# Performance work log

Measured on AMD Instinct MI355X. Metric: run time of the kernel, lower is better.

Reference implementation:

```python
import jax, jax.numpy as jnp
import numpy as np

B, T, IN_DIM = 128, 4096, 13
UNITS, MOTOR = 64, 6
LAYERS = [35, 23, 6]   # AutoNCP(64, 6): inter / command / motor neurons
_SPLITS = [35, 58]     # cumulative layer boundaries inside the 64-unit state


def setup_inputs() -> dict:
    keys = iter(jax.random.split(jax.random.key(0), 64))
    def rn(shape, s=0.1):
        return jax.random.normal(next(keys), shape, dtype=jnp.float32) * s
    inp = {"x": jax.random.normal(next(keys), (B, T, IN_DIM), dtype=jnp.float32)}
    # mixed-memory LSTM cell (ncps: input_map has bias, recurrent_map does not)
    inp["lstm_wi"] = rn((4 * UNITS, IN_DIM))
    inp["lstm_wh"] = rn((4 * UNITS, UNITS))
    inp["lstm_b"] = rn((4 * UNITS,))
    # wired CfC layers: ff1/ff2/time_a/time_b acting on concat([input, h])
    in_dims = [IN_DIM] + LAYERS[:-1]
    for i, (d, h) in enumerate(zip(in_dims, LAYERS)):
        for nm in ("w1", "w2", "wa", "wb"):
            inp[f"cfc{i}_{nm}"] = rn((h, d + h))
        for nm in ("b1", "b2", "ba", "bb"):
            inp[f"cfc{i}_{nm}"] = rn((h,))
    inp["gyro_w1"] = rn((32, MOTOR)); inp["gyro_b1"] = rn((32,))
    inp["gyro_w2"] = rn((3, 32));     inp["gyro_b2"] = rn((3,))
    inp["acc_w1"] = rn((32, MOTOR));  inp["acc_b1"] = rn((32,))
    inp["acc_w2"] = rn((3, 32));      inp["acc_b2"] = rn((3,))
    inp["unc_w1"] = rn((16, MOTOR));  inp["unc_b1"] = rn((16,))
    inp["unc_w2"] = rn((6, 16));      inp["unc_b2"] = rn((6,))
    return inp


def _cfc_step(inp, h, p):
    """ncps CfCCell, mode='default', no backbone, ts = 1.0."""
    W1, b1, W2, b2, Wa, ba, Wb, bb = p
    z = jnp.concatenate([inp, h], axis=-1)            # (B, in+hid)
    ff1 = jnp.tanh(z @ W1.T + b1)
    ff2 = jnp.tanh(z @ W2.T + b2)
    t = jax.nn.sigmoid((z @ Wa.T + ba) + (z @ Wb.T + bb))  # t_a*ts + t_b, ts==1
    return ff1 * (1.0 - t) + t * ff2


def reference(x, lstm_wi, lstm_wh, lstm_b,
              cfc0_w1, cfc0_b1, cfc0_w2, cfc0_b2, cfc0_wa, cfc0_ba, cfc0_wb, cfc0_bb,
              cfc1_w1, cfc1_b1, cfc1_w2, cfc1_b2, cfc1_wa, cfc1_ba, cfc1_wb, cfc1_bb,
              cfc2_w1, cfc2_b1, cfc2_w2, cfc2_b2, cfc2_wa, cfc2_ba, cfc2_wb, cfc2_bb,
              gyro_w1, gyro_b1, gyro_w2, gyro_b2,
              acc_w1, acc_b1, acc_w2, acc_b2,
              unc_w1, unc_b1, unc_w2, unc_b2):
    layer_params = (
        (cfc0_w1, cfc0_b1, cfc0_w2, cfc0_b2, cfc0_wa, cfc0_ba, cfc0_wb, cfc0_bb),
        (cfc1_w1, cfc1_b1, cfc1_w2, cfc1_b2, cfc1_wa, cfc1_ba, cfc1_wb, cfc1_bb),
        (cfc2_w1, cfc2_b1, cfc2_w2, cfc2_b2, cfc2_wa, cfc2_ba, cfc2_wb, cfc2_bb),
    )

    def step(carry, xt):  # xt: (B, 13)
        h, c = carry
        # mixed-memory LSTM over the full 64-unit state (forget gate +1.0)
        zg = xt @ lstm_wi.T + lstm_b + h @ lstm_wh.T
        ia, ig, fg, og = jnp.split(zg, 4, axis=-1)
        c_new = c * jax.nn.sigmoid(fg + 1.0) + jnp.tanh(ia) * jax.nn.sigmoid(ig)
        h_lstm = jnp.tanh(c_new) * jax.nn.sigmoid(og)
        # wired CfC: inter -> command -> motor, each fed previous layer's output
        hs = jnp.split(h_lstm, _SPLITS, axis=-1)
        inp = xt
        new_hs = []
        for hi, p in zip(hs, layer_params):
            inp = _cfc_step(inp, hi, p)
            new_hs.append(inp)
        return (jnp.concatenate(new_hs, axis=-1), c_new), inp  # motor out (B,6)

    Bsz = x.shape[0]
    h0 = jnp.zeros((Bsz, UNITS), x.dtype)
    c0 = jnp.zeros((Bsz, UNITS), x.dtype)
    _, outs = jax.lax.scan(step, (h0, c0), jnp.swapaxes(x, 0, 1))
    cfc_out = jnp.swapaxes(outs, 0, 1)  # (B, T, 6)

    gyro = jnp.tanh(cfc_out @ gyro_w1.T + gyro_b1) @ gyro_w2.T + gyro_b2
    acc = jnp.tanh(cfc_out @ acc_w1.T + acc_b1) @ acc_w2.T + acc_b2
    pred = jnp.concatenate([gyro, acc], axis=-1)                      # (B, T, 6)
    unc = jax.nn.softplus(
        jax.nn.relu(cfc_out @ unc_w1.T + unc_b1) @ unc_w2.T + unc_b2)  # (B, T, 6)
    return pred, unc
```

## Files before the change

### kernel.cpp

```cpp
#include <hip/hip_runtime.h>
#include <math.h>

#define BATCH 128
#define TSTEPS 4096
#define INDIM 13


__device__ __forceinline__ float fsig(float x) {
    return __builtin_amdgcn_rcpf(1.f + __expf(-x));
}
__device__ __forceinline__ float ftanh(float x) {
    float s = fsig(x + x);
    return s + s - 1.f;
}
__device__ __forceinline__ float fsoftplus(float x) {
    return (x > 15.f) ? x : __logf(1.f + __expf(x));
}

__device__ __forceinline__ float qxor1(float v) {
    return __int_as_float(__builtin_amdgcn_update_dpp(
        0, __float_as_int(v), 0xB1, 0xF, 0xF, true));
}
__device__ __forceinline__ float qxor2(float v) {
    return __int_as_float(__builtin_amdgcn_update_dpp(
        0, __float_as_int(v), 0x4E, 0xF, 0xF, true));
}
__device__ __forceinline__ float sxor4(float v) {
    return __int_as_float(__builtin_amdgcn_ds_swizzle(
        __float_as_int(v), 0x101F));
}
#define BFLY8(a) { a += sxor4(a); a += qxor2(a); a += qxor1(a); }

#define FMA4(acc, W, q, zv) { acc += zv.x * W##_##q##_0; acc += zv.y * W##_##q##_1; \
                              acc += zv.z * W##_##q##_2; acc += zv.w * W##_##q##_3; }

__global__ __launch_bounds__(512, 2)
void rnn_kernel(const float* __restrict__ x,
                const float* __restrict__ lstm_wi, const float* __restrict__ lstm_wh,
                const float* __restrict__ lstm_b,
                const float* __restrict__ c0w1, const float* __restrict__ c0w2,
                const float* __restrict__ c0wa, const float* __restrict__ c0wb,
                const float* __restrict__ c0b1, const float* __restrict__ c0b2,
                const float* __restrict__ c0ba, const float* __restrict__ c0bb,
                const float* __restrict__ c1w1, const float* __restrict__ c1w2,
                const float* __restrict__ c1wa, const float* __restrict__ c1wb,
                const float* __restrict__ c1b1, const float* __restrict__ c1b2,
                const float* __restrict__ c1ba, const float* __restrict__ c1bb,
                const float* __restrict__ c2w1, const float* __restrict__ c2w2,
                const float* __restrict__ c2wa, const float* __restrict__ c2wb,
                const float* __restrict__ c2b1, const float* __restrict__ c2b2,
                const float* __restrict__ c2ba, const float* __restrict__ c2bb,
                float* __restrict__ out)
{
    const int bb = blockIdx.x;
    const int t  = threadIdx.x;
    const int k  = t & 7;
    const int u  = t >> 3;

    __shared__ __align__(16) float smem[256];
    float* zL = smem;
    float* z0 = smem + 96;
    float* z1 = smem + 160;
    float* z2 = smem + 224;

    const long xbase = (long)bb * TSTEPS * INDIM;
    const long obase = (long)bb * TSTEPS * 6;

    auto lwf = [&](int A, int c) -> float {
        int r = A * 64 + u;
        return (c < 13) ? lstm_wi[r * 13 + c]
             : (c < 77) ? lstm_wh[r * 64 + (c - 13)] : 0.f;
    };
#define DEF_WL(A,q) \
    float wl##A##_##q##_0 = lwf(A, 12*k + 4*q + 0); \
    float wl##A##_##q##_1 = lwf(A, 12*k + 4*q + 1); \
    float wl##A##_##q##_2 = lwf(A, 12*k + 4*q + 2); \
    float wl##A##_##q##_3 = lwf(A, 12*k + 4*q + 3);
    DEF_WL(0,0) DEF_WL(0,1) DEF_WL(0,2)
    DEF_WL(1,0) DEF_WL(1,1) DEF_WL(1,2)
    DEF_WL(2,0) DEF_WL(2,1) DEF_WL(2,2)
    DEF_WL(3,0) DEF_WL(3,1) DEF_WL(3,2)
#undef DEF_WL
    const float bL0 = lstm_b[u];
    const float bL1 = lstm_b[64 + u];
    const float bL2 = lstm_b[128 + u];
    const float bL3 = lstm_b[192 + u];

    const int grp  = (u < 35) ? 0 : (u < 58) ? 1 : 2;
    const int row  = (grp == 0) ? u : (grp == 1) ? (u - 35) : (u - 58);
    const int rl   = (grp == 0) ? 48 : (grp == 1) ? 58 : 29;
    const int clen = (grp == 2) ? 4 : 8;
    const int cb   = (grp == 2) ? 4 * k : 8 * k;
    const float *W0p, *W1p, *W2p, *W3p;
    float bC0, bC1, bC2, bC3;
    if (grp == 0) {
        W0p = c0w1 + row * 48; W1p = c0w2 + row * 48;
        W2p = c0wa + row * 48; W3p = c0wb + row * 48;
        bC0 = c0b1[row]; bC1 = c0b2[row]; bC2 = c0ba[row]; bC3 = c0bb[row];
    } else if (grp == 1) {
        W0p = c1w1 + row * 58; W1p = c1w2 + row * 58;
        W2p = c1wa + row * 58; W3p = c1wb + row * 58;
        bC0 = c1b1[row]; bC1 = c1b2[row]; bC2 = c1ba[row]; bC3 = c1bb[row];
    } else {
        W0p = c2w1 + row * 29; W1p = c2w2 + row * 29;
        W2p = c2wa + row * 29; W3p = c2wb + row * 29;
        bC0 = c2b1[row]; bC1 = c2b2[row]; bC2 = c2ba[row]; bC3 = c2bb[row];
    }
    auto cwf = [&](const float* W, int c) -> float {
        int cc = cb + c;
        return (c < clen && cc < rl) ? W[cc] : 0.f;
    };
#define DEF_WC(A,q) \
    float wc##A##_##q##_0 = cwf(W##A##p, 4*q + 0); \
    float wc##A##_##q##_1 = cwf(W##A##p, 4*q + 1); \
    float wc##A##_##q##_2 = cwf(W##A##p, 4*q + 2); \
    float wc##A##_##q##_3 = cwf(W##A##p, 4*q + 3);
    DEF_WC(0,0) DEF_WC(0,1)
    DEF_WC(1,0) DEF_WC(1,1)
    DEF_WC(2,0) DEF_WC(2,1)
    DEF_WC(3,0) DEF_WC(3,1)
#undef DEF_WC

    const bool pfl = (t >= 128 && t < 141);
    float creg = 0.f;

    if (t < 256) smem[t] = 0.f;
    __syncthreads();
    if (t < 13) zL[t] = x[xbase + t];
    __syncthreads();

    #pragma unroll 1
    for (int ts = 0; ts < TSTEPS; ++ts) {
        float xn = 0.f;
        if (pfl && (ts + 1) < TSTEPS)
            xn = x[xbase + (long)(ts + 1) * 13 + (t - 128)];
        if (t >= 256 && t < 269) z0[t - 256] = zL[t - 256];
        {
            const float4* zc = (const float4*)(zL + 12 * k);
            float4 q0 = zc[0], q1 = zc[1], q2 = zc[2];
            float a0 = 0.f, a1 = 0.f, a2 = 0.f, a3 = 0.f;
            FMA4(a0, wl0, 0, q0) FMA4(a0, wl0, 1, q1) FMA4(a0, wl0, 2, q2)
            FMA4(a1, wl1, 0, q0) FMA4(a1, wl1, 1, q1) FMA4(a1, wl1, 2, q2)
            FMA4(a2, wl2, 0, q0) FMA4(a2, wl2, 1, q1) FMA4(a2, wl2, 2, q2)
            FMA4(a3, wl3, 0, q0) FMA4(a3, wl3, 1, q1) FMA4(a3, wl3, 2, q2)
            BFLY8(a0) BFLY8(a1) BFLY8(a2) BFLY8(a3)
            a0 += bL0; a1 += bL1; a2 += bL2; a3 += bL3;
            float cn = creg * fsig(a2 + 1.f) + ftanh(a0) * fsig(a1);
            creg = cn;
            float hl = ftanh(cn) * fsig(a3);
            if (k == 0) {
                if (u < 35)      z0[13 + u] = hl;
                else if (u < 58) z1[u]      = hl;
                else             z2[u - 35] = hl;
            }
        }
        __syncthreads();

        if (grp == 0) {
            const float4* zc = (const float4*)(z0 + 8 * k);
            float4 p0 = zc[0], p1 = zc[1];
            float a0 = 0.f, a1 = 0.f, a2 = 0.f, a3 = 0.f;
            FMA4(a0, wc0, 0, p0) FMA4(a0, wc0, 1, p1)
            FMA4(a1, wc1, 0, p0) FMA4(a1, wc1, 1, p1)
            FMA4(a2, wc2, 0, p0) FMA4(a2, wc2, 1, p1)
            FMA4(a3, wc3, 0, p0) FMA4(a3, wc3, 1, p1)
            BFLY8(a0) BFLY8(a1) BFLY8(a2) BFLY8(a3)
            a0 += bC0; a1 += bC1; a2 += bC2; a3 += bC3;
            float tg = fsig(a2 + a3);
            float f1 = ftanh(a0), f2 = ftanh(a1);
            float o = f1 + tg * (f2 - f1);
            if (k == 0) { z1[row] = o; zL[13 + row] = o; }
        }
        __syncthreads();

        if (grp == 1) {
            const float4* zc = (const float4*)(z1 + 8 * k);
            float4 p0 = zc[0], p1 = zc[1];
            float a0 = 0.f, a1 = 0.f, a2 = 0.f, a3 = 0.f;
            FMA4(a0, wc0, 0, p0) FMA4(a0, wc0, 1, p1)
            FMA4(a1, wc1, 0, p0) FMA4(a1, wc1, 1, p1)
            FMA4(a2, wc2, 0, p0) FMA4(a2, wc2, 1, p1)
            FMA4(a3, wc3, 0, p0) FMA4(a3, wc3, 1, p1)
            BFLY8(a0) BFLY8(a1) BFLY8(a2) BFLY8(a3)
            a0 += bC0; a1 += bC1; a2 += bC2; a3 += bC3;
            float tg = fsig(a2 + a3);
            float f1 = ftanh(a0), f2 = ftanh(a1);
            float o = f1 + tg * (f2 - f1);
            if (k == 0) { z2[row] = o; zL[48 + row] = o; }
        }
        __syncthreads();

        if (grp == 2) {
            const float4* zc = (const float4*)(z2 + 4 * k);
            float4 p0 = zc[0];
            float a0 = 0.f, a1 = 0.f, a2 = 0.f, a3 = 0.f;
            FMA4(a0, wc0, 0, p0)
            FMA4(a1, wc1, 0, p0)
            FMA4(a2, wc2, 0, p0)
            FMA4(a3, wc3, 0, p0)
            BFLY8(a0) BFLY8(a1) BFLY8(a2) BFLY8(a3)
            a0 += bC0; a1 += bC1; a2 += bC2; a3 += bC3;
            float tg = fsig(a2 + a3);
            float f1 = ftanh(a0), f2 = ftanh(a1);
            float o = f1 + tg * (f2 - f1);
            if (k == 0) {
                out[obase + (long)ts * 6 + row] = o;
                zL[71 + row] = o;
            }
        } else if (pfl) {
            zL[t - 128] = xn;
        }
        __syncthreads();
    }
}

#define S_GW1 0
#define S_GB1 192
#define S_GW2 224
#define S_GB2 320
#define S_AW1 323
#define S_AB1 515
#define S_AW2 547
#define S_AB2 643
#define S_UW1 646
#define S_UB1 742
#define S_UW2 758
#define S_UB2 854
#define S_TOT 860

__global__ __launch_bounds__(256)
void head_kernel(const float* __restrict__ gw1, const float* __restrict__ gb1,
                 const float* __restrict__ gw2, const float* __restrict__ gb2,
                 const float* __restrict__ aw1, const float* __restrict__ ab1,
                 const float* __restrict__ aw2, const float* __restrict__ ab2,
                 const float* __restrict__ uw1, const float* __restrict__ ub1,
                 const float* __restrict__ uw2, const float* __restrict__ ub2,
                 float* __restrict__ out)
{
    __shared__ float s[S_TOT];
    const int t = threadIdx.x;
    if (t < 192) { s[S_GW1 + t] = gw1[t]; s[S_AW1 + t] = aw1[t]; }
    if (t < 96)  { s[S_GW2 + t] = gw2[t]; s[S_AW2 + t] = aw2[t];
                   s[S_UW1 + t] = uw1[t]; s[S_UW2 + t] = uw2[t]; }
    if (t < 32)  { s[S_GB1 + t] = gb1[t]; s[S_AB1 + t] = ab1[t]; }
    if (t < 16)  { s[S_UB1 + t] = ub1[t]; }
    if (t < 3)   { s[S_GB2 + t] = gb2[t]; s[S_AB2 + t] = ab2[t]; }
    if (t < 6)   { s[S_UB2 + t] = ub2[t]; }
    __syncthreads();

    const long p = (long)blockIdx.x * 256 + t;
    const long base = p * 6;
    float m0 = out[base+0], m1 = out[base+1], m2 = out[base+2];
    float m3 = out[base+3], m4 = out[base+4], m5 = out[base+5];

    float gy0 = s[S_GB2+0], gy1 = s[S_GB2+1], gy2 = s[S_GB2+2];
    float ac0 = s[S_AB2+0], ac1 = s[S_AB2+1], ac2 = s[S_AB2+2];
    #pragma unroll
    for (int i = 0; i < 32; ++i) {
        float hg = s[S_GB1+i] + s[S_GW1+i*6+0]*m0 + s[S_GW1+i*6+1]*m1
                 + s[S_GW1+i*6+2]*m2 + s[S_GW1+i*6+3]*m3
                 + s[S_GW1+i*6+4]*m4 + s[S_GW1+i*6+5]*m5;
        hg = ftanh(hg);
        gy0 += s[S_GW2+i]*hg; gy1 += s[S_GW2+32+i]*hg; gy2 += s[S_GW2+64+i]*hg;
        float ha = s[S_AB1+i] + s[S_AW1+i*6+0]*m0 + s[S_AW1+i*6+1]*m1
                 + s[S_AW1+i*6+2]*m2 + s[S_AW1+i*6+3]*m3
                 + s[S_AW1+i*6+4]*m4 + s[S_AW1+i*6+5]*m5;
        ha = ftanh(ha);
        ac0 += s[S_AW2+i]*ha; ac1 += s[S_AW2+32+i]*ha; ac2 += s[S_AW2+64+i]*ha;
    }
    float u0 = s[S_UB2+0], u1 = s[S_UB2+1], u2 = s[S_UB2+2];
    float u3 = s[S_UB2+3], u4 = s[S_UB2+4], u5 = s[S_UB2+5];
    #pragma unroll
    for (int i = 0; i < 16; ++i) {
        float hu = s[S_UB1+i] + s[S_UW1+i*6+0]*m0 + s[S_UW1+i*6+1]*m1
                 + s[S_UW1+i*6+2]*m2 + s[S_UW1+i*6+3]*m3
                 + s[S_UW1+i*6+4]*m4 + s[S_UW1+i*6+5]*m5;
        hu = fmaxf(hu, 0.f);
        u0 += s[S_UW2+i]*hu;      u1 += s[S_UW2+16+i]*hu; u2 += s[S_UW2+32+i]*hu;
        u3 += s[S_UW2+48+i]*hu;   u4 += s[S_UW2+64+i]*hu; u5 += s[S_UW2+80+i]*hu;
    }
    out[base+0] = gy0; out[base+1] = gy1; out[base+2] = gy2;
    out[base+3] = ac0; out[base+4] = ac1; out[base+5] = ac2;
    const long uoff = (long)BATCH * TSTEPS * 6;
    out[uoff+base+0] = fsoftplus(u0); out[uoff+base+1] = fsoftplus(u1);
    out[uoff+base+2] = fsoftplus(u2); out[uoff+base+3] = fsoftplus(u3);
    out[uoff+base+4] = fsoftplus(u4); out[uoff+base+5] = fsoftplus(u5);
}

extern "C" void kernel_launch(void* const* d_in, const int* in_sizes, int n_in,
                              void* d_out, int out_size, void* d_ws, size_t ws_size,
                              hipStream_t stream) {
    const float* x       = (const float*)d_in[0];
    const float* lstm_wi = (const float*)d_in[1];
    const float* lstm_wh = (const float*)d_in[2];
    const float* lstm_b  = (const float*)d_in[3];
    const float* c0w1 = (const float*)d_in[4];
    const float* c0w2 = (const float*)d_in[5];
    const float* c0wa = (const float*)d_in[6];
    const float* c0wb = (const float*)d_in[7];
    const float* c0b1 = (const float*)d_in[8];
    const float* c0b2 = (const float*)d_in[9];
    const float* c0ba = (const float*)d_in[10];
    const float* c0bb = (const float*)d_in[11];
    const float* c1w1 = (const float*)d_in[12];
    const float* c1w2 = (const float*)d_in[13];
    const float* c1wa = (const float*)d_in[14];
    const float* c1wb = (const float*)d_in[15];
    const float* c1b1 = (const float*)d_in[16];
    const float* c1b2 = (const float*)d_in[17];
    const float* c1ba = (const float*)d_in[18];
    const float* c1bb = (const float*)d_in[19];
    const float* c2w1 = (const float*)d_in[20];
    const float* c2w2 = (const float*)d_in[21];
    const float* c2wa = (const float*)d_in[22];
    const float* c2wb = (const float*)d_in[23];
    const float* c2b1 = (const float*)d_in[24];
    const float* c2b2 = (const float*)d_in[25];
    const float* c2ba = (const float*)d_in[26];
    const float* c2bb = (const float*)d_in[27];
    const float* gw1 = (const float*)d_in[28];
    const float* gb1 = (const float*)d_in[29];
    const float* gw2 = (const float*)d_in[30];
    const float* gb2 = (const float*)d_in[31];
    const float* aw1 = (const float*)d_in[32];
    const float* ab1 = (const float*)d_in[33];
    const float* aw2 = (const float*)d_in[34];
    const float* ab2 = (const float*)d_in[35];
    const float* uw1 = (const float*)d_in[36];
    const float* ub1 = (const float*)d_in[37];
    const float* uw2 = (const float*)d_in[38];
    const float* ub2 = (const float*)d_in[39];
    float* out = (float*)d_out;

    rnn_kernel<<<BATCH, 512, 0, stream>>>(x, lstm_wi, lstm_wh, lstm_b,
        c0w1, c0w2, c0wa, c0wb, c0b1, c0b2, c0ba, c0bb,
        c1w1, c1w2, c1wa, c1wb, c1b1, c1b2, c1ba, c1bb,
        c2w1, c2w2, c2wa, c2wb, c2b1, c2b2, c2ba, c2bb, out);

    head_kernel<<<(BATCH * TSTEPS) / 256, 256, 0, stream>>>(
        gw1, gb1, gw2, gb2, aw1, ab1, aw2, ab2, uw1, ub1, uw2, ub2, out);
}
```

Before: 5.845 ms.

## Park recurrent weights in AccVGPRs and use DPP row-mirror for reduction

Moves the per-thread LSTM and CfC weight and bias registers into accumulation VGPRs through inline asm, reading them back with v_accvgpr_read before each FMA. This frees architectural VGPRs so the 512-thread, 2-block launch bound can be met without spilling. It also swaps the ds_swizzle xor-4 step of the 8-lane butterfly for a DPP row half-mirror, keeping the whole reduction in DPP instead of going through the LDS crossbar, and it walks the x prefetch with a running pointer. The cost is an extra read instruction per weight use on every step, and volatile asm may prevent the compiler from scheduling these reads freely.

Measured after the change: 6.822 ms. 1.17x slower.

```diff
diff --git a/kernel.cpp b/kernel.cpp
--- a/kernel.cpp
+++ b/kernel.cpp
@@ -17,6 +17,17 @@
     return (x > 15.f) ? x : __logf(1.f + __expf(x));
 }
 
+__device__ __forceinline__ float apark(float v) {
+    float r;
+    asm volatile("v_accvgpr_write_b32 %0, %1" : "=a"(r) : "v"(v));
+    return r;
+}
+__device__ __forceinline__ float aread(float a) {
+    float r;
+    asm volatile("v_accvgpr_read_b32 %0, %1" : "=v"(r) : "a"(a));
+    return r;
+}
+
 __device__ __forceinline__ float qxor1(float v) {
     return __int_as_float(__builtin_amdgcn_update_dpp(
         0, __float_as_int(v), 0xB1, 0xF, 0xF, true));
@@ -25,14 +36,15 @@
     return __int_as_float(__builtin_amdgcn_update_dpp(
         0, __float_as_int(v), 0x4E, 0xF, 0xF, true));
 }
-__device__ __forceinline__ float sxor4(float v) {
-    return __int_as_float(__builtin_amdgcn_ds_swizzle(
-        __float_as_int(v), 0x101F));
-}
-#define BFLY8(a) { a += sxor4(a); a += qxor2(a); a += qxor1(a); }
-
-#define FMA4(acc, W, q, zv) { acc += zv.x * W##_##q##_0; acc += zv.y * W##_##q##_1; \
-                              acc += zv.z * W##_##q##_2; acc += zv.w * W##_##q##_3; }
+__device__ __forceinline__ float hmir(float v) {
+    return __int_as_float(__builtin_amdgcn_update_dpp(
+        0, __float_as_int(v), 0x141, 0xF, 0xF, true));
+}
+#define BFLY8(a) { a += qxor1(a); a += qxor2(a); a += hmir(a); }
+
+#define FMA4(acc, W, q, zv) { \
+    acc += aread(W##_##q##_0) * zv.x; acc += aread(W##_##q##_1) * zv.y; \
+    acc += aread(W##_##q##_2) * zv.z; acc += aread(W##_##q##_3) * zv.w; }
 
 __global__ __launch_bounds__(512, 2)
 void rnn_kernel(const float* __restrict__ x,
@@ -72,19 +84,19 @@
              : (c < 77) ? lstm_wh[r * 64 + (c - 13)] : 0.f;
     };
 #define DEF_WL(A,q) \
-    float wl##A##_##q##_0 = lwf(A, 12*k + 4*q + 0); \
-    float wl##A##_##q##_1 = lwf(A, 12*k + 4*q + 1); \
-    float wl##A##_##q##_2 = lwf(A, 12*k + 4*q + 2); \
-    float wl##A##_##q##_3 = lwf(A, 12*k + 4*q + 3);
+    float wl##A##_##q##_0 = apark(lwf(A, 12*k + 4*q + 0)); \
+    float wl##A##_##q##_1 = apark(lwf(A, 12*k + 4*q + 1)); \
+    float wl##A##_##q##_2 = apark(lwf(A, 12*k + 4*q + 2)); \
+    float wl##A##_##q##_3 = apark(lwf(A, 12*k + 4*q + 3));
     DEF_WL(0,0) DEF_WL(0,1) DEF_WL(0,2)
     DEF_WL(1,0) DEF_WL(1,1) DEF_WL(1,2)
     DEF_WL(2,0) DEF_WL(2,1) DEF_WL(2,2)
     DEF_WL(3,0) DEF_WL(3,1) DEF_WL(3,2)
 #undef DEF_WL
-    const float bL0 = lstm_b[u];
-    const float bL1 = lstm_b[64 + u];
-    const float bL2 = lstm_b[128 + u];
-    const float bL3 = lstm_b[192 + u];
+    const float bL0 = apark(lstm_b[u]);
+    const float bL1 = apark(lstm_b[64 + u]);
+    const float bL2 = apark(lstm_b[128 + u]);
+    const float bL3 = apark(lstm_b[192 + u]);
 
     const int grp  = (u < 35) ? 0 : (u < 58) ? 1 : 2;
     const int row  = (grp == 0) ? u : (grp == 1) ? (u - 35) : (u - 58);
@@ -92,29 +104,31 @@
     const int clen = (grp == 2) ? 4 : 8;
     const int cb   = (grp == 2) ? 4 * k : 8 * k;
     const float *W0p, *W1p, *W2p, *W3p;
-    float bC0, bC1, bC2, bC3;
+    float bC0r, bC1r, bC2r, bC3r;
     if (grp == 0) {
         W0p = c0w1 + row * 48; W1p = c0w2 + row * 48;
         W2p = c0wa + row * 48; W3p = c0wb + row * 48;
-        bC0 = c0b1[row]; bC1 = c0b2[row]; bC2 = c0ba[row]; bC3 = c0bb[row];
+        bC0r = c0b1[row]; bC1r = c0b2[row]; bC2r = c0ba[row]; bC3r = c0bb[row];
     } else if (grp == 1) {
         W0p = c1w1 + row * 58; W1p = c1w2 + row * 58;
         W2p = c1wa + row * 58; W3p = c1wb + row * 58;
-        bC0 = c1b1[row]; bC1 = c1b2[row]; bC2 = c1ba[row]; bC3 = c1bb[row];
+        bC0r = c1b1[row]; bC1r = c1b2[row]; bC2r = c1ba[row]; bC3r = c1bb[row];
     } else {
         W0p = c2w1 + row * 29; W1p = c2w2 + row * 29;
         W2p = c2wa + row * 29; W3p = c2wb + row * 29;
-        bC0 = c2b1[row]; bC1 = c2b2[row]; bC2 = c2ba[row]; bC3 = c2bb[row];
+        bC0r = c2b1[row]; bC1r = c2b2[row]; bC2r = c2ba[row]; bC3r = c2bb[row];
     }
+    const float bC0 = apark(bC0r), bC1 = apark(bC1r);
+    const float bC2 = apark(bC2r), bC3 = apark(bC3r);
     auto cwf = [&](const float* W, int c) -> float {
         int cc = cb + c;
         return (c < clen && cc < rl) ? W[cc] : 0.f;
     };
 #define DEF_WC(A,q) \
-    float wc##A##_##q##_0 = cwf(W##A##p, 4*q + 0); \
-    float wc##A##_##q##_1 = cwf(W##A##p, 4*q + 1); \
-    float wc##A##_##q##_2 = cwf(W##A##p, 4*q + 2); \
-    float wc##A##_##q##_3 = cwf(W##A##p, 4*q + 3);
+    float wc##A##_##q##_0 = apark(cwf(W##A##p, 4*q + 0)); \
+    float wc##A##_##q##_1 = apark(cwf(W##A##p, 4*q + 1)); \
+    float wc##A##_##q##_2 = apark(cwf(W##A##p, 4*q + 2)); \
+    float wc##A##_##q##_3 = apark(cwf(W##A##p, 4*q + 3));
     DEF_WC(0,0) DEF_WC(0,1)
     DEF_WC(1,0) DEF_WC(1,1)
     DEF_WC(2,0) DEF_WC(2,1)
@@ -123,6 +137,7 @@
 
     const bool pfl = (t >= 128 && t < 141);
     float creg = 0.f;
+    const float* xs = x + xbase + 13;
 
     if (t < 256) smem[t] = 0.f;
     __syncthreads();
@@ -132,8 +147,7 @@
     #pragma unroll 1
     for (int ts = 0; ts < TSTEPS; ++ts) {
         float xn = 0.f;
-        if (pfl && (ts + 1) < TSTEPS)
-            xn = x[xbase + (long)(ts + 1) * 13 + (t - 128)];
+        if (pfl && (ts + 1) < TSTEPS) xn = xs[t - 128];
         if (t >= 256 && t < 269) z0[t - 256] = zL[t - 256];
         {
             const float4* zc = (const float4*)(zL + 12 * k);
@@ -144,7 +158,8 @@
             FMA4(a2, wl2, 0, q0) FMA4(a2, wl2, 1, q1) FMA4(a2, wl2, 2, q2)
             FMA4(a3, wl3, 0, q0) FMA4(a3, wl3, 1, q1) FMA4(a3, wl3, 2, q2)
             BFLY8(a0) BFLY8(a1) BFLY8(a2) BFLY8(a3)
-            a0 += bL0; a1 += bL1; a2 += bL2; a3 += bL3;
+            a0 += aread(bL0); a1 += aread(bL1);
+            a2 += aread(bL2); a3 += aread(bL3);
             float cn = creg * fsig(a2 + 1.f) + ftanh(a0) * fsig(a1);
             creg = cn;
             float hl = ftanh(cn) * fsig(a3);
@@ -165,7 +180,8 @@
             FMA4(a2, wc2, 0, p0) FMA4(a2, wc2, 1, p1)
             FMA4(a3, wc3, 0, p0) FMA4(a3, wc3, 1, p1)
             BFLY8(a0) BFLY8(a1) BFLY8(a2) BFLY8(a3)
-            a0 += bC0; a1 += bC1; a2 += bC2; a3 += bC3;
+            a0 += aread(bC0); a1 += aread(bC1);
+            a2 += aread(bC2); a3 += aread(bC3);
             float tg = fsig(a2 + a3);
             float f1 = ftanh(a0), f2 = ftanh(a1);
             float o = f1 + tg * (f2 - f1);
@@ -182,7 +198,8 @@
             FMA4(a2, wc2, 0, p0) FMA4(a2, wc2, 1, p1)
             FMA4(a3, wc3, 0, p0) FMA4(a3, wc3, 1, p1)
             BFLY8(a0) BFLY8(a1) BFLY8(a2) BFLY8(a3)
-            a0 += bC0; a1 += bC1; a2 += bC2; a3 += bC3;
+            a0 += aread(bC0); a1 += aread(bC1);
+            a2 += aread(bC2); a3 += aread(bC3);
             float tg = fsig(a2 + a3);
             float f1 = ftanh(a0), f2 = ftanh(a1);
             float o = f1 + tg * (f2 - f1);
@@ -199,7 +216,8 @@
             FMA4(a2, wc2, 0, p0)
             FMA4(a3, wc3, 0, p0)
             BFLY8(a0) BFLY8(a1) BFLY8(a2) BFLY8(a3)
-            a0 += bC0; a1 += bC1; a2 += bC2; a3 += bC3;
+            a0 += aread(bC0); a1 += aread(bC1);
+            a2 += aread(bC2); a3 += aread(bC3);
             float tg = fsig(a2 + a3);
             float f1 = ftanh(a0), f2 = ftanh(a1);
             float o = f1 + tg * (f2 - f1);
@@ -211,6 +229,7 @@
             zL[t - 128] = xn;
         }
         __syncthreads();
+        xs += 13;
     }
 }
 
```

## Precompute LSTM partial sums early and move side traffic off critical phases

Applied to the files above, without the earlier changes.

The LSTM gate dot products for the parts of the input/state vector that are already final (x and the first layers' outputs) are now computed at the end of the previous step, before the last barrier. Only the motor-layer entries are accumulated at the start of the next step. The x prefetch and output stores move to threads that are idle during the CfC phases, and the output write is delayed one step. The 8-lane butterfly now uses a DPP row-half-mirror instead of ds_swizzle. This shortens the serial critical path of each timestep, at the cost of more branching by k and keeping four partial-sum registers live across the step.

Measured after the change: 6.385 ms. 1.09x slower.

```diff
diff --git a/kernel.cpp b/kernel.cpp
--- a/kernel.cpp
+++ b/kernel.cpp
@@ -25,14 +25,32 @@
     return __int_as_float(__builtin_amdgcn_update_dpp(
         0, __float_as_int(v), 0x4E, 0xF, 0xF, true));
 }
-__device__ __forceinline__ float sxor4(float v) {
-    return __int_as_float(__builtin_amdgcn_ds_swizzle(
-        __float_as_int(v), 0x101F));
-}
-#define BFLY8(a) { a += sxor4(a); a += qxor2(a); a += qxor1(a); }
+__device__ __forceinline__ float hmir(float v) {
+    return __int_as_float(__builtin_amdgcn_update_dpp(
+        0, __float_as_int(v), 0x141, 0xF, 0xF, true));
+}
+#define BFLY8(a) { a += qxor1(a); a += qxor2(a); a += hmir(a); }
 
 #define FMA4(acc, W, q, zv) { acc += zv.x * W##_##q##_0; acc += zv.y * W##_##q##_1; \
                               acc += zv.z * W##_##q##_2; acc += zv.w * W##_##q##_3; }
+
+#define LPART() { \
+    p0 = 0.f; p1 = 0.f; p2 = 0.f; p3 = 0.f; \
+    if (k < 5) { \
+        const float4* zc = (const float4*)(zL + 12 * k); \
+        float4 q0 = zc[0], q1 = zc[1], q2 = zc[2]; \
+        FMA4(p0, wl0, 0, q0) FMA4(p0, wl0, 1, q1) FMA4(p0, wl0, 2, q2) \
+        FMA4(p1, wl1, 0, q0) FMA4(p1, wl1, 1, q1) FMA4(p1, wl1, 2, q2) \
+        FMA4(p2, wl2, 0, q0) FMA4(p2, wl2, 1, q1) FMA4(p2, wl2, 2, q2) \
+        FMA4(p3, wl3, 0, q0) FMA4(p3, wl3, 1, q1) FMA4(p3, wl3, 2, q2) \
+    } else if (k == 5) { \
+        const float4* zc = (const float4*)(zL + 60); \
+        float4 q0 = zc[0], q1 = zc[1]; \
+        FMA4(p0, wl0, 0, q0) FMA4(p0, wl0, 1, q1) \
+        FMA4(p1, wl1, 0, q0) FMA4(p1, wl1, 1, q1) \
+        FMA4(p2, wl2, 0, q0) FMA4(p2, wl2, 1, q1) \
+        FMA4(p3, wl3, 0, q0) FMA4(p3, wl3, 1, q1) \
+    } }
 
 __global__ __launch_bounds__(512, 2)
 void rnn_kernel(const float* __restrict__ x,
@@ -121,7 +139,10 @@
     DEF_WC(3,0) DEF_WC(3,1)
 #undef DEF_WC
 
-    const bool pfl = (t >= 128 && t < 141);
+    const bool cpx = (t >= 256 && t < 269);
+    const bool stl = (t >= 320 && t < 326);
+    const bool pfl = (t >= 328 && t < 341);
+
     float creg = 0.f;
 
     if (t < 256) smem[t] = 0.f;
@@ -129,20 +150,25 @@
     if (t < 13) zL[t] = x[xbase + t];
     __syncthreads();
 
+    float p0, p1, p2, p3;
+    LPART();
+
     #pragma unroll 1
     for (int ts = 0; ts < TSTEPS; ++ts) {
-        float xn = 0.f;
-        if (pfl && (ts + 1) < TSTEPS)
-            xn = x[xbase + (long)(ts + 1) * 13 + (t - 128)];
-        if (t >= 256 && t < 269) z0[t - 256] = zL[t - 256];
         {
-            const float4* zc = (const float4*)(zL + 12 * k);
-            float4 q0 = zc[0], q1 = zc[1], q2 = zc[2];
-            float a0 = 0.f, a1 = 0.f, a2 = 0.f, a3 = 0.f;
-            FMA4(a0, wl0, 0, q0) FMA4(a0, wl0, 1, q1) FMA4(a0, wl0, 2, q2)
-            FMA4(a1, wl1, 0, q0) FMA4(a1, wl1, 1, q1) FMA4(a1, wl1, 2, q2)
-            FMA4(a2, wl2, 0, q0) FMA4(a2, wl2, 1, q1) FMA4(a2, wl2, 2, q2)
-            FMA4(a3, wl3, 0, q0) FMA4(a3, wl3, 1, q1) FMA4(a3, wl3, 2, q2)
+            float a0 = p0, a1 = p1, a2 = p2, a3 = p3;
+            if (k == 5) {
+                float4 v = *(const float4*)(zL + 68);
+                FMA4(a0, wl0, 2, v) FMA4(a1, wl1, 2, v)
+                FMA4(a2, wl2, 2, v) FMA4(a3, wl3, 2, v)
+            } else if (k == 6) {
+                const float4* zc = (const float4*)(zL + 72);
+                float4 v0 = zc[0], v1 = zc[1];
+                FMA4(a0, wl0, 0, v0) FMA4(a0, wl0, 1, v1)
+                FMA4(a1, wl1, 0, v0) FMA4(a1, wl1, 1, v1)
+                FMA4(a2, wl2, 0, v0) FMA4(a2, wl2, 1, v1)
+                FMA4(a3, wl3, 0, v0) FMA4(a3, wl3, 1, v1)
+            }
             BFLY8(a0) BFLY8(a1) BFLY8(a2) BFLY8(a3)
             a0 += bL0; a1 += bL1; a2 += bL2; a3 += bL3;
             float cn = creg * fsig(a2 + 1.f) + ftanh(a0) * fsig(a1);
@@ -153,17 +179,23 @@
                 else if (u < 58) z1[u]      = hl;
                 else             z2[u - 35] = hl;
             }
+            if (cpx) z0[t - 256] = zL[t - 256];
         }
         __syncthreads();
 
+        float xn = 0.f;
+        if (pfl && (ts + 1) < TSTEPS)
+            xn = x[xbase + (long)(ts + 1) * 13 + (t - 328)];
+        if (stl && ts > 0)
+            out[obase + (long)(ts - 1) * 6 + (t - 320)] = zL[71 + (t - 320)];
         if (grp == 0) {
             const float4* zc = (const float4*)(z0 + 8 * k);
-            float4 p0 = zc[0], p1 = zc[1];
+            float4 v0 = zc[0], v1 = zc[1];
             float a0 = 0.f, a1 = 0.f, a2 = 0.f, a3 = 0.f;
-            FMA4(a0, wc0, 0, p0) FMA4(a0, wc0, 1, p1)
-            FMA4(a1, wc1, 0, p0) FMA4(a1, wc1, 1, p1)
-            FMA4(a2, wc2, 0, p0) FMA4(a2, wc2, 1, p1)
-            FMA4(a3, wc3, 0, p0) FMA4(a3, wc3, 1, p1)
+            FMA4(a0, wc0, 0, v0) FMA4(a0, wc0, 1, v1)
+            FMA4(a1, wc1, 0, v0) FMA4(a1, wc1, 1, v1)
+            FMA4(a2, wc2, 0, v0) FMA4(a2, wc2, 1, v1)
+            FMA4(a3, wc3, 0, v0) FMA4(a3, wc3, 1, v1)
             BFLY8(a0) BFLY8(a1) BFLY8(a2) BFLY8(a3)
             a0 += bC0; a1 += bC1; a2 += bC2; a3 += bC3;
             float tg = fsig(a2 + a3);
@@ -173,14 +205,15 @@
         }
         __syncthreads();
 
+        if (pfl) zL[t - 328] = xn;
         if (grp == 1) {
             const float4* zc = (const float4*)(z1 + 8 * k);
-            float4 p0 = zc[0], p1 = zc[1];
+            float4 v0 = zc[0], v1 = zc[1];
             float a0 = 0.f, a1 = 0.f, a2 = 0.f, a3 = 0.f;
-            FMA4(a0, wc0, 0, p0) FMA4(a0, wc0, 1, p1)
-            FMA4(a1, wc1, 0, p0) FMA4(a1, wc1, 1, p1)
-            FMA4(a2, wc2, 0, p0) FMA4(a2, wc2, 1, p1)
-            FMA4(a3, wc3, 0, p0) FMA4(a3, wc3, 1, p1)
+            FMA4(a0, wc0, 0, v0) FMA4(a0, wc0, 1, v1)
+            FMA4(a1, wc1, 0, v0) FMA4(a1, wc1, 1, v1)
+            FMA4(a2, wc2, 0, v0) FMA4(a2, wc2, 1, v1)
+            FMA4(a3, wc3, 0, v0) FMA4(a3, wc3, 1, v1)
             BFLY8(a0) BFLY8(a1) BFLY8(a2) BFLY8(a3)
             a0 += bC0; a1 += bC1; a2 += bC2; a3 += bC3;
             float tg = fsig(a2 + a3);
@@ -192,26 +225,24 @@
 
         if (grp == 2) {
             const float4* zc = (const float4*)(z2 + 4 * k);
-            float4 p0 = zc[0];
+            float4 v0 = zc[0];
             float a0 = 0.f, a1 = 0.f, a2 = 0.f, a3 = 0.f;
-            FMA4(a0, wc0, 0, p0)
-            FMA4(a1, wc1, 0, p0)
-            FMA4(a2, wc2, 0, p0)
-            FMA4(a3, wc3, 0, p0)
+            FMA4(a0, wc0, 0, v0)
+            FMA4(a1, wc1, 0, v0)
+            FMA4(a2, wc2, 0, v0)
+            FMA4(a3, wc3, 0, v0)
             BFLY8(a0) BFLY8(a1) BFLY8(a2) BFLY8(a3)
             a0 += bC0; a1 += bC1; a2 += bC2; a3 += bC3;
             float tg = fsig(a2 + a3);
             float f1 = ftanh(a0), f2 = ftanh(a1);
             float o = f1 + tg * (f2 - f1);
-            if (k == 0) {
-                out[obase + (long)ts * 6 + row] = o;
-                zL[71 + row] = o;
-            }
-        } else if (pfl) {
-            zL[t - 128] = xn;
+            if (k == 0) zL[71 + row] = o;
         }
+        LPART();
         __syncthreads();
     }
+
+    if (t < 6) out[obase + (long)(TSTEPS - 1) * 6 + t] = zL[71 + t];
 }
 
 #define S_GW1 0
```

## Stage input and output in double-buffered LDS tiles and use DPP row-mirror reduction

Applied to the files above, without the earlier changes.

Replaces the per-step global load of the next x row and the per-step global store of motor outputs with 64-step tiles staged in shared memory. Idle threads bulk-load the next x tile with float4 loads and flush finished output tiles with float4 stores, both double-buffered. This takes global-memory latency out of the serial recurrence. The 8-lane butterfly also swaps the ds_swizzle for a DPP half-row mirror, cutting LDS traffic in the reduction. In exchange, shared memory grows to about 10.5 KB, and the index arithmetic (the thread offset, the unaligned float4 access on x) adds correctness risk.

Measured after the change: 5.453 ms. 6.7% less time.

```diff
diff --git a/kernel.cpp b/kernel.cpp
--- a/kernel.cpp
+++ b/kernel.cpp
@@ -4,6 +4,7 @@
 #define BATCH 128
 #define TSTEPS 4096
 #define INDIM 13
+#define XT 64
 
 
 __device__ __forceinline__ float fsig(float x) {
@@ -25,11 +26,11 @@
     return __int_as_float(__builtin_amdgcn_update_dpp(
         0, __float_as_int(v), 0x4E, 0xF, 0xF, true));
 }
-__device__ __forceinline__ float sxor4(float v) {
-    return __int_as_float(__builtin_amdgcn_ds_swizzle(
-        __float_as_int(v), 0x101F));
-}
-#define BFLY8(a) { a += sxor4(a); a += qxor2(a); a += qxor1(a); }
+__device__ __forceinline__ float hmir(float v) {
+    return __int_as_float(__builtin_amdgcn_update_dpp(
+        0, __float_as_int(v), 0x141, 0xF, 0xF, true));
+}
+#define BFLY8(a) { a += qxor1(a); a += qxor2(a); a += hmir(a); }
 
 #define FMA4(acc, W, q, zv) { acc += zv.x * W##_##q##_0; acc += zv.y * W##_##q##_1; \
                               acc += zv.z * W##_##q##_2; acc += zv.w * W##_##q##_3; }
@@ -57,11 +58,15 @@
     const int k  = t & 7;
     const int u  = t >> 3;
 
-    __shared__ __align__(16) float smem[256];
-    float* zL = smem;
-    float* z0 = smem + 96;
-    float* z1 = smem + 160;
-    float* z2 = smem + 224;
+    __shared__ __align__(16) float smem[2688];
+    float* zL  = smem;
+    float* z0  = smem + 96;
+    float* z1  = smem + 160;
+    float* z2  = smem + 224;
+    float* xt0 = smem + 256;
+    float* xt1 = smem + 1088;
+    float* ot0 = smem + 1920;
+    float* ot1 = smem + 2304;
 
     const long xbase = (long)bb * TSTEPS * INDIM;
     const long obase = (long)bb * TSTEPS * 6;
@@ -121,19 +126,21 @@
     DEF_WC(3,0) DEF_WC(3,1)
 #undef DEF_WC
 
-    const bool pfl = (t >= 128 && t < 141);
     float creg = 0.f;
 
     if (t < 256) smem[t] = 0.f;
-    __syncthreads();
+    if (t < 208) {
+        float4 xi = *(const float4*)(x + xbase + 4 * t);
+        *(float4*)&xt0[4 * t] = xi;
+    }
     if (t < 13) zL[t] = x[xbase + t];
     __syncthreads();
 
     #pragma unroll 1
     for (int ts = 0; ts < TSTEPS; ++ts) {
-        float xn = 0.f;
-        if (pfl && (ts + 1) < TSTEPS)
-            xn = x[xbase + (long)(ts + 1) * 13 + (t - 128)];
+        const int par = (ts >> 6) & 1;
+        const int lts = ts & 63;
+
         if (t >= 256 && t < 269) z0[t - 256] = zL[t - 256];
         {
             const float4* zc = (const float4*)(zL + 12 * k);
@@ -158,29 +165,46 @@
 
         if (grp == 0) {
             const float4* zc = (const float4*)(z0 + 8 * k);
-            float4 p0 = zc[0], p1 = zc[1];
+            float4 v0 = zc[0], v1 = zc[1];
             float a0 = 0.f, a1 = 0.f, a2 = 0.f, a3 = 0.f;
-            FMA4(a0, wc0, 0, p0) FMA4(a0, wc0, 1, p1)
-            FMA4(a1, wc1, 0, p0) FMA4(a1, wc1, 1, p1)
-            FMA4(a2, wc2, 0, p0) FMA4(a2, wc2, 1, p1)
-            FMA4(a3, wc3, 0, p0) FMA4(a3, wc3, 1, p1)
+            FMA4(a0, wc0, 0, v0) FMA4(a0, wc0, 1, v1)
+            FMA4(a1, wc1, 0, v0) FMA4(a1, wc1, 1, v1)
+            FMA4(a2, wc2, 0, v0) FMA4(a2, wc2, 1, v1)
+            FMA4(a3, wc3, 0, v0) FMA4(a3, wc3, 1, v1)
             BFLY8(a0) BFLY8(a1) BFLY8(a2) BFLY8(a3)
             a0 += bC0; a1 += bC1; a2 += bC2; a3 += bC3;
             float tg = fsig(a2 + a3);
             float f1 = ftanh(a0), f2 = ftanh(a1);
             float o = f1 + tg * (f2 - f1);
             if (k == 0) { z1[row] = o; zL[13 + row] = o; }
+        } else {
+            if (lts == 62 && (ts + 2) < TSTEPS) {
+                int i = t - 280;
+                if (i < 208) {
+                    float4 v = *(const float4*)(x + xbase + (long)(ts + 2) * 13 + 4 * i);
+                    float* dst = par ? xt0 : xt1;
+                    *(float4*)&dst[4 * i] = v;
+                }
+            }
+            if (lts == 0 && ts > 0) {
+                int i = t - 280;
+                if (i < 96) {
+                    const float* src = par ? ot0 : ot1;
+                    float4 v = *(const float4*)&src[4 * i];
+                    *(float4*)(out + obase + (long)(ts - XT) * 6 + 4 * i) = v;
+                }
+            }
         }
         __syncthreads();
 
         if (grp == 1) {
             const float4* zc = (const float4*)(z1 + 8 * k);
-            float4 p0 = zc[0], p1 = zc[1];
+            float4 v0 = zc[0], v1 = zc[1];
             float a0 = 0.f, a1 = 0.f, a2 = 0.f, a3 = 0.f;
-            FMA4(a0, wc0, 0, p0) FMA4(a0, wc0, 1, p1)
-            FMA4(a1, wc1, 0, p0) FMA4(a1, wc1, 1, p1)
-            FMA4(a2, wc2, 0, p0) FMA4(a2, wc2, 1, p1)
-            FMA4(a3, wc3, 0, p0) FMA4(a3, wc3, 1, p1)
+            FMA4(a0, wc0, 0, v0) FMA4(a0, wc0, 1, v1)
+            FMA4(a1, wc1, 0, v0) FMA4(a1, wc1, 1, v1)
+            FMA4(a2, wc2, 0, v0) FMA4(a2, wc2, 1, v1)
+            FMA4(a3, wc3, 0, v0) FMA4(a3, wc3, 1, v1)
             BFLY8(a0) BFLY8(a1) BFLY8(a2) BFLY8(a3)
             a0 += bC0; a1 += bC1; a2 += bC2; a3 += bC3;
             float tg = fsig(a2 + a3);
@@ -192,25 +216,35 @@
 
         if (grp == 2) {
             const float4* zc = (const float4*)(z2 + 4 * k);
-            float4 p0 = zc[0];
+            float4 v0 = zc[0];
             float a0 = 0.f, a1 = 0.f, a2 = 0.f, a3 = 0.f;
-            FMA4(a0, wc0, 0, p0)
-            FMA4(a1, wc1, 0, p0)
-            FMA4(a2, wc2, 0, p0)
-            FMA4(a3, wc3, 0, p0)
+            FMA4(a0, wc0, 0, v0)
+            FMA4(a1, wc1, 0, v0)
+            FMA4(a2, wc2, 0, v0)
+            FMA4(a3, wc3, 0, v0)
             BFLY8(a0) BFLY8(a1) BFLY8(a2) BFLY8(a3)
             a0 += bC0; a1 += bC1; a2 += bC2; a3 += bC3;
             float tg = fsig(a2 + a3);
             float f1 = ftanh(a0), f2 = ftanh(a1);
             float o = f1 + tg * (f2 - f1);
             if (k == 0) {
-                out[obase + (long)ts * 6 + row] = o;
                 zL[71 + row] = o;
+                float* ob = par ? ot1 : ot0;
+                ob[lts * 6 + row] = o;
             }
-        } else if (pfl) {
-            zL[t - 128] = xn;
+        } else if (t < 13 && (ts + 1) < TSTEPS) {
+            const float* xb = (((ts + 1) >> 6) & 1) ? xt1 : xt0;
+            zL[t] = xb[((ts + 1) & 63) * 13 + t];
         }
         __syncthreads();
+    }
+
+    {
+        int i = t - 280;
+        if (i >= 0 && i < 96) {
+            float4 v = *(const float4*)&ot1[4 * i];
+            *(float4*)(out + obase + (long)(TSTEPS - XT) * 6 + 4 * i) = v;
+        }
     }
 }
 
```
